# Kernel tuning notes

Hardware: AMD Instinct MI355X
Metric: run time of the kernel (lower is better)

The kernel has to match this reference:

```python
import jax, jax.numpy as jnp
import numpy as np

N, E, T, D, A = 16384, 65536, 2048, 64, 6


def _w(k, shape, fan_in):
    return jax.random.normal(k, shape, jnp.float32) / np.sqrt(fan_in)


def setup_inputs() -> dict:
    key = jax.random.key(0)
    ks = jax.random.split(key, 20)
    inp = {}
    inp["x"] = jax.random.normal(ks[0], (N, 3), jnp.float32)
    inp["edge_attr"] = jax.random.normal(ks[1], (E, 7), jnp.float32)
    inp["edge_index"] = jax.random.randint(ks[2], (2, E), 0, N)
    inp["nonring"] = jax.random.randint(ks[3], (T, 4), 0, N)
    inp["hx"] = jnp.zeros((1, D), jnp.float32)
    inp["cx"] = jnp.zeros((1, D), jnp.float32)
    inp["W_lin0"] = _w(ks[4], (D, 3), 3); inp["b_lin0"] = jnp.zeros((D,), jnp.float32)
    inp["W_e1"] = _w(ks[5], (128, 7), 7); inp["b_e1"] = jnp.zeros((128,), jnp.float32)
    inp["W_e2"] = _w(ks[6], (D * D, 128), 128); inp["b_e2"] = jnp.zeros((D * D,), jnp.float32)
    inp["conv_root"] = _w(ks[7], (D, D), D); inp["conv_bias"] = jnp.zeros((D,), jnp.float32)
    inp["gru_Wih"] = _w(ks[8], (3 * D, D), D); inp["gru_Whh"] = _w(ks[9], (3 * D, D), D)
    inp["gru_bih"] = jnp.zeros((3 * D,), jnp.float32); inp["gru_bhh"] = jnp.zeros((3 * D,), jnp.float32)
    inp["s2s_Wih"] = _w(ks[10], (4 * D, 2 * D), 2 * D); inp["s2s_Whh"] = _w(ks[11], (4 * D, D), D)
    inp["s2s_bih"] = jnp.zeros((4 * D,), jnp.float32); inp["s2s_bhh"] = jnp.zeros((4 * D,), jnp.float32)
    inp["mem_Wih"] = _w(ks[12], (4 * D, 2 * D), 2 * D); inp["mem_Whh"] = _w(ks[13], (4 * D, D), D)
    inp["mem_bih"] = jnp.zeros((4 * D,), jnp.float32); inp["mem_bhh"] = jnp.zeros((4 * D,), jnp.float32)
    inp["W_lin1"] = _w(ks[14], (D, 5 * D), 5 * D); inp["b_lin1"] = jnp.zeros((D,), jnp.float32)
    inp["W_lin2"] = _w(ks[15], (A, D), D); inp["b_lin2"] = jnp.zeros((A,), jnp.float32)
    inp["W_lin3"] = _w(ks[16], (1, 3 * D), 3 * D); inp["b_lin3"] = jnp.zeros((1,), jnp.float32)
    return inp


def _lstm_cell(xin, h, c, Wih, Whh, bih, bhh):
    g = xin @ Wih.T + bih + h @ Whh.T + bhh
    i, f, gg, o = jnp.split(g, 4, axis=-1)  # torch gate order i,f,g,o
    c = jax.nn.sigmoid(f) * c + jax.nn.sigmoid(i) * jnp.tanh(gg)
    h = jax.nn.sigmoid(o) * jnp.tanh(c)
    return h, c


def _gru_cell(xin, h, Wih, Whh, bih, bhh):
    gi = xin @ Wih.T + bih
    gh = h @ Whh.T + bhh
    ir, iz, inn = jnp.split(gi, 3, axis=-1)  # torch gate order r,z,n
    hr, hz, hn = jnp.split(gh, 3, axis=-1)
    r = jax.nn.sigmoid(ir + hr)
    z = jax.nn.sigmoid(iz + hz)
    n = jnp.tanh(inn + r * hn)
    return (1.0 - z) * n + z * h


def reference(x, edge_attr, edge_index, nonring, hx, cx,
              W_lin0, b_lin0, W_e1, b_e1, W_e2, b_e2, conv_root, conv_bias,
              gru_Wih, gru_Whh, gru_bih, gru_bhh,
              s2s_Wih, s2s_Whh, s2s_bih, s2s_bhh,
              mem_Wih, mem_Whh, mem_bih, mem_bhh,
              W_lin1, b_lin1, W_lin2, b_lin2, W_lin3, b_lin3):
    src, tgt = edge_index[0], edge_index[1]
    out = jax.nn.relu(x @ W_lin0.T + b_lin0)  # [N, D]
    h = out  # GRU hidden (nodes as batch)
    # edge-conditioned dim x dim matrices (NNConv edge MLP)
    ew = jax.nn.relu(edge_attr @ W_e1.T + b_e1)
    ew = (ew @ W_e2.T + b_e2).reshape(E, D, D)  # [E, D, D]
    cnt = jnp.maximum(jax.ops.segment_sum(jnp.ones((E,), out.dtype), tgt, num_segments=N), 1.0)
    for _ in range(3):
        msg = jnp.einsum('ed,edf->ef', out[src], ew)  # per-edge small matmul
        aggr = jax.ops.segment_sum(msg, tgt, num_segments=N) / cnt[:, None]  # scatter-mean
        m = jax.nn.relu(aggr + out @ conv_root + conv_bias)  # NNConv root + bias, then relu
        h = _gru_cell(m, h, gru_Wih, gru_Whh, gru_bih, gru_bhh)
        out = h
    # Set2Set pooling (single graph, B=1), processing_steps=3
    hs = jnp.zeros((1, D), out.dtype)
    cs = jnp.zeros((1, D), out.dtype)
    q_star = jnp.zeros((1, 2 * D), out.dtype)
    for _ in range(3):
        hs, cs = _lstm_cell(q_star, hs, cs, s2s_Wih, s2s_Whh, s2s_bih, s2s_bhh)
        a = jax.nn.softmax(out @ hs[0])  # [N]
        r = (a[:, None] * out).sum(0, keepdims=True)  # [1, D]
        q_star = jnp.concatenate([hs, r], axis=1)
    pool = q_star  # [1, 2D]
    lstm_out, cx_new = _lstm_cell(pool, hx, cx, mem_Wih, mem_Whh, mem_bih, mem_bhh)
    hx_new = lstm_out
    # torsion head: index_select -> view(4*D, -1) -> permute(1,0)
    sel = out[nonring.reshape(-1)]  # [4T, D]
    tfeat = sel.reshape(4 * D, -1).T  # [T, 4D], faithful to torch view semantics
    rep = jnp.repeat(lstm_out.reshape(-1), T).reshape(T, D)  # torch repeat_interleave + view
    pf = jnp.concatenate([tfeat, rep], axis=1)  # [T, 5D]
    logits = jax.nn.relu(pf @ W_lin1.T + b_lin1) @ W_lin2.T + b_lin2  # [T, A]
    v = jnp.concatenate([pool, lstm_out], axis=1) @ W_lin3.T + b_lin3  # [1, 1]
    return logits, v, hx_new, cx_new
```

## Files before the change

kernel.cpp:

```cpp
#include <hip/hip_runtime.h>

#define cN 16384
#define cE 65536
#define cT 2048
#define CAP 78

typedef __attribute__((ext_vector_type(8))) short short8;
typedef __attribute__((ext_vector_type(4))) float f32x4;
typedef __attribute__((ext_vector_type(4))) unsigned u32x4;

__device__ __forceinline__ short f2bf(float f){
  unsigned u = __float_as_uint(f);
  u = (u + 0x7FFFu + ((u >> 16) & 1u)) >> 16;
  return (short)u;
}
__device__ __forceinline__ float bf2f(short s){
  return __uint_as_float(((unsigned)(unsigned short)s) << 16);
}
__device__ __forceinline__ unsigned cvtpk(float lo, float hi){
  unsigned r;
  asm("v_cvt_pk_bf16_f32 %0, %1, %2" : "=v"(r) : "v"(lo), "v"(hi));
  return r;
}
__device__ __forceinline__ float sigm(float x){ return 1.f / (1.f + __expf(-x)); }
__device__ __forceinline__ unsigned fenc(float f){
  unsigned u = __float_as_uint(f);
  return (u & 0x80000000u) ? ~u : (u | 0x80000000u);
}
__device__ __forceinline__ float fdec(unsigned u){
  u = (u & 0x80000000u) ? (u & 0x7FFFFFFFu) : ~u;
  return __uint_as_float(u);
}
__device__ __forceinline__ float wred(float v){
  v += __shfl_xor(v, 32); v += __shfl_xor(v, 16); v += __shfl_xor(v, 8);
  v += __shfl_xor(v, 4);  v += __shfl_xor(v, 2);  v += __shfl_xor(v, 1);
  return v;
}

__global__ __launch_bounds__(256) void k_lin0(const float* __restrict__ x,
    const float* __restrict__ W, const float* __restrict__ b, float* __restrict__ out)
{
  int i = blockIdx.x * 256 + threadIdx.x;
  int n = i >> 6, f = i & 63;
  float acc = b[f] + x[n*3]*W[f*3] + x[n*3+1]*W[f*3+1] + x[n*3+2]*W[f*3+2];
  out[i] = fmaxf(acc, 0.f);
}

__global__ __launch_bounds__(256) void k_h1(const float* __restrict__ ea,
    const float* __restrict__ W, const float* __restrict__ b, short* __restrict__ h1)
{
  int i = blockIdx.x * 256 + threadIdx.x;
  int e = i >> 7, k = i & 127;
  const float* a = ea + e * 7;
  const float* w = W + k * 7;
  float acc = b[k];
  #pragma unroll
  for (int c = 0; c < 7; c++) acc += a[c] * w[c];
  h1[i] = f2bf(fmaxf(acc, 0.f));
}

__global__ __launch_bounds__(256) void k_w2f(const float* __restrict__ W2, short* __restrict__ w2f)
{
  int o = blockIdx.x * 256 + threadIdx.x;
  int j = o & 7, l = (o >> 3) & 63, ks = (o >> 9) & 31, c = (o >> 14) & 7, fb = (o >> 17) & 3;
  int f = fb * 16 + (l & 15);
  int d = c * 8 + j;
  int k = ks * 4 + ((l >> 4) & 3);
  w2f[o] = f2bf(W2[(d * 64 + f) * 128 + k]);
}

__global__ __launch_bounds__(256) void k_b2f(const float* __restrict__ b2, short* __restrict__ b2f)
{
  int o = blockIdx.x * 256 + threadIdx.x;
  int j = o & 7, l = (o >> 3) & 63, ks2 = (o >> 9) & 1, fb = (o >> 10) & 3;
  int d = ks2 * 32 + ((l >> 4) & 3) * 8 + j;
  int f = fb * 16 + (l & 15);
  b2f[o] = f2bf(b2[d * 64 + f]);
}

__global__ __launch_bounds__(256) void k_wpack(const float* __restrict__ convW,
    const float* __restrict__ Wih, const float* __restrict__ Whh, short* __restrict__ wpk)
{
  int o = blockIdx.x * 256 + threadIdx.x;
  int j = o & 7, l = (o >> 3) & 63, kc = (o >> 9) & 1, cb = o >> 10;
  int k = kc * 32 + ((l >> 4) & 3) * 8 + j;
  int c16 = l & 15;
  float v;
  if (cb < 4)       v = convW[k * 64 + cb * 16 + c16];
  else if (cb < 16) v = Wih[((cb - 4) * 16 + c16) * 64 + k];
  else              v = Whh[((cb - 16) * 16 + c16) * 64 + k];
  wpk[o] = f2bf(v);
}

__global__ __launch_bounds__(256) void k_deg(const int* __restrict__ ei, int* __restrict__ deg)
{
  int e = blockIdx.x * 256 + threadIdx.x;
  atomicAdd(&deg[ei[cE + e]], 1);
}

__global__ __launch_bounds__(1024) void k_scan(const int* __restrict__ deg,
    int* __restrict__ rowp, float* __restrict__ cnt)
{
  __shared__ int part[1024];
  int tid = threadIdx.x;
  int base = tid * 16;
  int loc[16]; int s = 0;
  #pragma unroll
  for (int i = 0; i < 16; i++){ loc[i] = s; s += deg[base + i]; }
  part[tid] = s;
  __syncthreads();
  for (int off = 1; off < 1024; off <<= 1){
    int v = (tid >= off) ? part[tid - off] : 0;
    __syncthreads();
    part[tid] += v;
    __syncthreads();
  }
  int inc = part[tid];
  int eb = inc - s;
  #pragma unroll
  for (int i = 0; i < 16; i++){
    rowp[base + i] = eb + loc[i];
    int dv = deg[base + i];
    cnt[base + i] = (float)(dv > 0 ? dv : 1);
  }
  if (tid == 1023) rowp[16384] = inc;
}

__global__ __launch_bounds__(256) void k_scatter(const int* __restrict__ ei,
    const int* __restrict__ rowp, int* __restrict__ cur,
    int* __restrict__ esrc, int* __restrict__ eidx)
{
  int e = blockIdx.x * 256 + threadIdx.x;
  int t = ei[cE + e];
  int pos = rowp[t] + atomicAdd(&cur[t], 1);
  esrc[pos] = ei[e];
  eidx[pos] = e;
}

__global__ __launch_bounds__(256) void k_sagg(const float* __restrict__ out,
    const short* __restrict__ h1, const short* __restrict__ w2f,
    const short* __restrict__ b2f, const int* __restrict__ rowp,
    const int* __restrict__ esrc, const int* __restrict__ eidx,
    float* __restrict__ aggr)
{
  __shared__ __align__(16) short S[16][1040];
  __shared__ __align__(16) unsigned h1i[CAP][64];
  __shared__ __align__(16) float outsf[CAP][64];
  __shared__ __align__(16) short osb[16][72];
  int tid = threadIdx.x, w = tid >> 6, lane = tid & 63;
  int t0 = blockIdx.x * 16;

  int ebase = rowp[t0];
  int eend  = rowp[t0 + 16];
  int ecnt  = eend - ebase;
  bool fits = (ecnt <= CAP);
  int scnt  = fits ? ecnt : CAP;
  for (int i = w; i < scnt; i += 4){
    int eid = eidx[ebase + i];
    int src = esrc[ebase + i];
    unsigned lo = (unsigned short)h1[(size_t)eid * 128 + lane];
    unsigned hi = (unsigned short)h1[(size_t)eid * 128 + 64 + lane];
    h1i[i][lane] = lo | (hi << 16);
    outsf[i][lane] = out[(size_t)src * 64 + lane];
  }
  int toff[4], tcnt[4];
  #pragma unroll
  for (int g = 0; g < 4; g++){
    int t = t0 + w * 4 + g;
    int a = rowp[t], b = rowp[t + 1];
    toff[g] = a - ebase; tcnt[g] = b - a;
  }
  __syncthreads();

  #pragma unroll
  for (int g = 0; g < 4; g++){
    int ti = w * 4 + g;
    float os = 0.f;
    int tf = toff[g], tc = tcnt[g];
    for (int p = 0; p < tc; p++){
      int slot = tf + p;
      if (slot < CAP) os += outsf[slot][lane];
      else            os += out[(size_t)esrc[ebase + slot] * 64 + lane];
    }
    osb[ti][lane] = (short)cvtpk(os, os);
  }

  f32x4 acc = {0.f, 0.f, 0.f, 0.f};
  int arow = lane & 15, kg = lane >> 4;
  for (int c = 0; c < 8; ++c){
    #pragma unroll
    for (int g = 0; g < 4; ++g){
      int ti = w * 4 + g;
      float a0[8], a1[8];
      #pragma unroll
      for (int d = 0; d < 8; d++){ a0[d] = 0.f; a1[d] = 0.f; }
      int tc = tcnt[g], tf = toff[g];
      if (fits){
        #pragma unroll 2
        for (int p = 0; p < tc; ++p){
          int slot = tf + p;
          unsigned u = h1i[slot][lane];
          float h1a = __uint_as_float(u << 16);
          float h1b = __uint_as_float(u & 0xFFFF0000u);
          f32x4 o0 = *(const f32x4*)&outsf[slot][c * 8];
          f32x4 o1 = *(const f32x4*)&outsf[slot][c * 8 + 4];
          a0[0] = fmaf(o0[0], h1a, a0[0]); a1[0] = fmaf(o0[0], h1b, a1[0]);
          a0[1] = fmaf(o0[1], h1a, a0[1]); a1[1] = fmaf(o0[1], h1b, a1[1]);
          a0[2] = fmaf(o0[2], h1a, a0[2]); a1[2] = fmaf(o0[2], h1b, a1[2]);
          a0[3] = fmaf(o0[3], h1a, a0[3]); a1[3] = fmaf(o0[3], h1b, a1[3]);
          a0[4] = fmaf(o1[0], h1a, a0[4]); a1[4] = fmaf(o1[0], h1b, a1[4]);
          a0[5] = fmaf(o1[1], h1a, a0[5]); a1[5] = fmaf(o1[1], h1b, a1[5]);
          a0[6] = fmaf(o1[2], h1a, a0[6]); a1[6] = fmaf(o1[2], h1b, a1[6]);
          a0[7] = fmaf(o1[3], h1a, a0[7]); a1[7] = fmaf(o1[3], h1b, a1[7]);
        }
      } else {
        for (int p = 0; p < tc; ++p){
          int slot = tf + p;
          float h1a, h1b;
          if (slot < CAP){
            unsigned u = h1i[slot][lane];
            h1a = __uint_as_float(u << 16);
            h1b = __uint_as_float(u & 0xFFFF0000u);
            f32x4 o0 = *(const f32x4*)&outsf[slot][c * 8];
            f32x4 o1 = *(const f32x4*)&outsf[slot][c * 8 + 4];
            #pragma unroll
            for (int d = 0; d < 4; d++){
              a0[d] = fmaf(o0[d], h1a, a0[d]); a1[d] = fmaf(o0[d], h1b, a1[d]);
              a0[4+d] = fmaf(o1[d], h1a, a0[4+d]); a1[4+d] = fmaf(o1[d], h1b, a1[4+d]);
            }
          } else {
            int eid = eidx[ebase + slot];
            int src = esrc[ebase + slot];
            h1a = bf2f(h1[(size_t)eid * 128 + lane]);
            h1b = bf2f(h1[(size_t)eid * 128 + 64 + lane]);
            #pragma unroll
            for (int d = 0; d < 8; d++){
              float o = out[(size_t)src * 64 + c * 8 + d];
              a0[d] = fmaf(o, h1a, a0[d]); a1[d] = fmaf(o, h1b, a1[d]);
            }
          }
        }
      }
      u32x4 p0, p1;
      p0[0] = cvtpk(a0[0], a0[1]); p0[1] = cvtpk(a0[2], a0[3]);
      p0[2] = cvtpk(a0[4], a0[5]); p0[3] = cvtpk(a0[6], a0[7]);
      p1[0] = cvtpk(a1[0], a1[1]); p1[1] = cvtpk(a1[2], a1[3]);
      p1[2] = cvtpk(a1[4], a1[5]); p1[3] = cvtpk(a1[6], a1[7]);
      *(u32x4*)&S[ti][lane * 8]       = p0;
      *(u32x4*)&S[ti][512 + lane * 8] = p1;
    }
    __syncthreads();
    const short* bbase = w2f + ((size_t)(w * 8 + c) * 32) * 512 + lane * 8;
    #pragma unroll
    for (int ks = 0; ks < 32; ++ks){
      short8 afr = *(const short8*)&S[arow][ks * 32 + kg * 8];
      short8 bfr = *(const short8*)(bbase + (size_t)ks * 512);
      acc = __builtin_amdgcn_mfma_f32_16x16x32_bf16(afr, bfr, acc, 0, 0, 0);
    }
    __syncthreads();
  }
  #pragma unroll
  for (int ks2 = 0; ks2 < 2; ++ks2){
    short8 osf = *(const short8*)&osb[arow][ks2 * 32 + kg * 8];
    short8 bfr = *(const short8*)(b2f + ((size_t)((w * 2 + ks2) * 64 + lane)) * 8);
    acc = __builtin_amdgcn_mfma_f32_16x16x32_bf16(osf, bfr, acc, 0, 0, 0);
  }
  int fcol = w * 16 + arow;
  int trow = kg * 4;
  #pragma unroll
  for (int q = 0; q < 4; q++)
    aggr[(size_t)(t0 + trow + q) * 64 + fcol] = acc[q];
}

__global__ __launch_bounds__(256) void k_nodeM(float* __restrict__ out,
    const float* __restrict__ aggr, const float* __restrict__ cnt,
    const short* __restrict__ wpk, const float* __restrict__ convB,
    const float* __restrict__ bih, const float* __restrict__ bhh)
{
  __shared__ __align__(16) short outA[64][72];
  __shared__ __align__(16) short mA[64][72];
  __shared__ float sb[448];
  const short8* WF = (const short8*)wpk;
  int tid = threadIdx.x, w = tid >> 6, lane = tid & 63;
  int n0 = blockIdx.x * 64;
  for (int i = tid; i < 2048; i += 256){
    int r = i >> 5, c2 = (i & 31) * 2;
    float2 v = *(const float2*)&out[(size_t)(n0 + r) * 64 + c2];
    *(unsigned*)&outA[r][c2] = cvtpk(v.x, v.y);
  }
  if (tid < 64) sb[tid] = convB[tid];
  for (int i = tid; i < 192; i += 256){ sb[64 + i] = bih[i]; sb[256 + i] = bhh[i]; }
  __syncthreads();
  int arow = lane & 15, kg = lane >> 4;
  int r0 = w * 16;
  short8 aof0 = *(const short8*)&outA[r0 + arow][kg * 8];
  short8 aof1 = *(const short8*)&outA[r0 + arow][32 + kg * 8];
  float ic[4];
  #pragma unroll
  for (int q = 0; q < 4; q++)
    ic[q] = 1.0f / fmaxf(cnt[n0 + r0 + kg * 4 + q], 1.0f);
  #pragma unroll
  for (int cf = 0; cf < 4; cf++){
    f32x4 a = {0.f, 0.f, 0.f, 0.f};
    a = __builtin_amdgcn_mfma_f32_16x16x32_bf16(aof0, WF[(cf * 2 + 0) * 64 + lane], a, 0, 0, 0);
    a = __builtin_amdgcn_mfma_f32_16x16x32_bf16(aof1, WF[(cf * 2 + 1) * 64 + lane], a, 0, 0, 0);
    int col = cf * 16 + arow;
    float cb_ = sb[col];
    #pragma unroll
    for (int q = 0; q < 4; q++){
      int r = n0 + r0 + kg * 4 + q;
      float m = fmaxf(aggr[(size_t)r * 64 + col] * ic[q] + a[q] + cb_, 0.f);
      mA[r0 + kg * 4 + q][col] = f2bf(m);
    }
  }
  __syncthreads();
  short8 amf0 = *(const short8*)&mA[r0 + arow][kg * 8];
  short8 amf1 = *(const short8*)&mA[r0 + arow][32 + kg * 8];
  #pragma unroll
  for (int co = 0; co < 4; co++){
    f32x4 gir = {0,0,0,0}, giz = {0,0,0,0}, gin = {0,0,0,0};
    f32x4 ghr = {0,0,0,0}, ghz = {0,0,0,0}, ghn = {0,0,0,0};
    gir = __builtin_amdgcn_mfma_f32_16x16x32_bf16(amf0, WF[((4  + co) * 2 + 0) * 64 + lane], gir, 0, 0, 0);
    gir = __builtin_amdgcn_mfma_f32_16x16x32_bf16(amf1, WF[((4  + co) * 2 + 1) * 64 + lane], gir, 0, 0, 0);
    giz = __builtin_amdgcn_mfma_f32_16x16x32_bf16(amf0, WF[((8  + co) * 2 + 0) * 64 + lane], giz, 0, 0, 0);
    giz = __builtin_amdgcn_mfma_f32_16x16x32_bf16(amf1, WF[((8  + co) * 2 + 1) * 64 + lane], giz, 0, 0, 0);
    gin = __builtin_amdgcn_mfma_f32_16x16x32_bf16(amf0, WF[((12 + co) * 2 + 0) * 64 + lane], gin, 0, 0, 0);
    gin = __builtin_amdgcn_mfma_f32_16x16x32_bf16(amf1, WF[((12 + co) * 2 + 1) * 64 + lane], gin, 0, 0, 0);
    ghr = __builtin_amdgcn_mfma_f32_16x16x32_bf16(aof0, WF[((16 + co) * 2 + 0) * 64 + lane], ghr, 0, 0, 0);
    ghr = __builtin_amdgcn_mfma_f32_16x16x32_bf16(aof1, WF[((16 + co) * 2 + 1) * 64 + lane], ghr, 0, 0, 0);
    ghz = __builtin_amdgcn_mfma_f32_16x16x32_bf16(aof0, WF[((20 + co) * 2 + 0) * 64 + lane], ghz, 0, 0, 0);
    ghz = __builtin_amdgcn_mfma_f32_16x16x32_bf16(aof1, WF[((20 + co) * 2 + 1) * 64 + lane], ghz, 0, 0, 0);
    ghn = __builtin_amdgcn_mfma_f32_16x16x32_bf16(aof0, WF[((24 + co) * 2 + 0) * 64 + lane], ghn, 0, 0, 0);
    ghn = __builtin_amdgcn_mfma_f32_16x16x32_bf16(aof1, WF[((24 + co) * 2 + 1) * 64 + lane], ghn, 0, 0, 0);
    int col = co * 16 + arow;
    float bir = sb[64 + col],  biz = sb[128 + col], bin_ = sb[192 + col];
    float bhr = sb[256 + col], bhz = sb[320 + col], bhn = sb[384 + col];
    #pragma unroll
    for (int q = 0; q < 4; q++){
      size_t r = (size_t)(n0 + r0 + kg * 4 + q);
      float rr = sigm(gir[q] + bir + ghr[q] + bhr);
      float zz = sigm(giz[q] + biz + ghz[q] + bhz);
      float nn = tanhf(gin[q] + bin_ + rr * (ghn[q] + bhn));
      float o = out[r * 64 + col];
      out[r * 64 + col] = (1.f - zz) * nn + zz * o;
    }
  }
}

__global__ __launch_bounds__(256) void k_dotsF(const float* __restrict__ out,
    const float* __restrict__ Wih, const float* __restrict__ Whh,
    const float* __restrict__ bih, const float* __restrict__ bhh,
    float* __restrict__ scal, float* __restrict__ sbuf, int st)
{
  __shared__ float q[128];
  __shared__ float hsL[64];
  __shared__ float gsh[4][64];
  __shared__ float hsh[64];
  __shared__ float smax[4];
  const float* pg = scal + st * 256;
  float* pn = scal + (st + 1) * 256;
  int tid = threadIdx.x, gg = tid >> 6, lane = tid & 63;
  if (gg == 0){
    float hs = pg[lane];
    float es = pg[193];
    float rv = (es == 0.f) ? 0.f : pg[128 + lane] / es;
    q[lane] = hs; q[64 + lane] = rv; hsL[lane] = hs;
  }
  __syncthreads();
  float2 fq = *(const float2*)&q[2 * lane];
  float hv0 = hsL[lane];
  #pragma unroll 4
  for (int o = 0; o < 64; o++){
    int row = gg * 64 + o;
    float2 wv = *(const float2*)&Wih[(size_t)row * 128 + 2 * lane];
    float s = wv.x * fq.x + wv.y * fq.y + Whh[(size_t)row * 64 + lane] * hv0;
    s = wred(s);
    if (lane == 0) gsh[gg][o] = s;
  }
  __syncthreads();
  if (gg == 0){
    float gi = gsh[0][lane] + bih[lane]       + bhh[lane];
    float gf = gsh[1][lane] + bih[64 + lane]  + bhh[64 + lane];
    float gv = gsh[2][lane] + bih[128 + lane] + bhh[128 + lane];
    float go = gsh[3][lane] + bih[192 + lane] + bhh[192 + lane];
    float cs = pg[64 + lane];
    float cn = sigm(gf) * cs + sigm(gi) * tanhf(gv);
    float hn = sigm(go) * tanhf(cn);
    hsh[lane] = hn;
    if (blockIdx.x == 0){ pn[lane] = hn; pn[64 + lane] = cn; }
  }
  __syncthreads();
  int nbase = blockIdx.x * 64 + gg * 16;
  float hv = hsh[lane];
  float wmax = -3.4e38f;
  #pragma unroll 4
  for (int i = 0; i < 16; i++){
    int n = nbase + i;
    float p = wred(out[(size_t)n * 64 + lane] * hv);
    if (lane == 0) sbuf[n] = p;
    wmax = fmaxf(wmax, p);
  }
  if (lane == 0) smax[gg] = wmax;
  __syncthreads();
  if (tid == 0){
    float m = fmaxf(fmaxf(smax[0], smax[1]), fmaxf(smax[2], smax[3]));
    atomicMax((unsigned*)(pn + 192), fenc(m));
  }
}

__global__ __launch_bounds__(256) void k_smF(const float* __restrict__ out,
    const float* __restrict__ sbuf, float* __restrict__ scal, int st)
{
  float* pn = scal + (st + 1) * 256;
  __shared__ float ebuf[64];
  __shared__ float rpart[4][64];
  int tid = threadIdx.x, wid = tid >> 6, lane = tid & 63;
  float gm = fdec(((const unsigned*)pn)[192]);
  int n0 = blockIdx.x * 64;
  if (tid < 64) ebuf[tid] = __expf(sbuf[n0 + tid] - gm);
  __syncthreads();
  float racc = 0.f;
  #pragma unroll 4
  for (int i = 0; i < 16; i++){
    int idx = wid * 16 + i;
    racc += ebuf[idx] * out[(size_t)(n0 + idx) * 64 + lane];
  }
  rpart[wid][lane] = racc;
  __syncthreads();
  if (wid == 0){
    float rt = rpart[0][lane] + rpart[1][lane] + rpart[2][lane] + rpart[3][lane];
    atomicAdd(&pn[128 + lane], rt);
  } else if (wid == 1){
    float es = wred(ebuf[lane]);
    if (lane == 0) atomicAdd(&pn[193], es);
  }
}

__global__ __launch_bounds__(256) void k_memlstm(const float* __restrict__ Wih,
    const float* __restrict__ Whh, const float* __restrict__ bih,
    const float* __restrict__ bhh, const float* __restrict__ hx,
    const float* __restrict__ cx, const float* __restrict__ W3,
    const float* __restrict__ b3, float* __restrict__ scal, float* __restrict__ dout)
{
  __shared__ float pool[128];
  __shared__ float hxs[64];
  __shared__ float gsh[4][64];
  __shared__ float lob[64];
  const float* pg = scal + 3 * 256;
  int tid = threadIdx.x, gg = tid >> 6, lane = tid & 63;
  if (gg == 0){
    pool[lane] = pg[lane];
    pool[64 + lane] = pg[128 + lane] / pg[193];
    hxs[lane] = hx[lane];
  }
  __syncthreads();
  float2 fq = *(const float2*)&pool[2 * lane];
  float hv = hxs[lane];
  #pragma unroll 4
  for (int o = 0; o < 64; o++){
    int row = gg * 64 + o;
    float2 wv = *(const float2*)&Wih[(size_t)row * 128 + 2 * lane];
    float s = wv.x * fq.x + wv.y * fq.y + Whh[(size_t)row * 64 + lane] * hv;
    s = wred(s);
    if (lane == 0) gsh[gg][o] = s;
  }
  __syncthreads();
  if (gg == 0){
    float gi = gsh[0][lane] + bih[lane]       + bhh[lane];
    float gf = gsh[1][lane] + bih[64 + lane]  + bhh[64 + lane];
    float gv = gsh[2][lane] + bih[128 + lane] + bhh[128 + lane];
    float go = gsh[3][lane] + bih[192 + lane] + bhh[192 + lane];
    float cn = sigm(gf) * cx[lane] + sigm(gi) * tanhf(gv);
    float hn = sigm(go) * tanhf(cn);
    dout[12289 + lane] = hn;
    dout[12353 + lane] = cn;
    scal[1024 + lane] = hn;
    lob[lane] = hn;
  }
  __syncthreads();
  if (gg == 0){
    float a = pool[lane] * W3[lane] + pool[64 + lane] * W3[64 + lane]
            + lob[lane] * W3[128 + lane];
    a = wred(a);
    if (lane == 0) dout[12288] = a + b3[0];
  }
}

__global__ __launch_bounds__(256) void k_head(const float* __restrict__ out,
    const int* __restrict__ nr, const float* __restrict__ scal,
    const float* __restrict__ W1, const float* __restrict__ b1,
    const float* __restrict__ W2, const float* __restrict__ b2,
    float* __restrict__ dout)
{
  __shared__ float pf[4][320];
  __shared__ float hb[4][64];
  int tid = threadIdx.x, wid = tid >> 6, lane = tid & 63;
  int t = blockIdx.x * 4 + wid;
  float lo = scal[1024 + (t >> 5)];
  #pragma unroll
  for (int rep = 0; rep < 4; rep++){
    int j = rep * 64 + lane;
    int idx = nr[j * 32 + (t >> 6)];
    pf[wid][j] = out[idx * 64 + (t & 63)];
  }
  pf[wid][256 + lane] = lo;
  __syncthreads();
  float acc = b1[lane];
  const float* w = W1 + lane * 320;
  #pragma unroll 4
  for (int j = 0; j < 320; j++) acc += pf[wid][j] * w[j];
  hb[wid][lane] = fmaxf(acc, 0.f);
  __syncthreads();
  if (lane < 6){
    float a2 = b2[lane];
    const float* w2 = W2 + lane * 64;
    #pragma unroll 4
    for (int f = 0; f < 64; f++) a2 += hb[wid][f] * w2[f];
    dout[t * 6 + lane] = a2;
  }
}

extern "C" void kernel_launch(void* const* d_in, const int* in_sizes, int n_in,
                              void* d_out, int out_size, void* d_ws, size_t ws_size,
                              hipStream_t stream)
{
  const float* x         = (const float*)d_in[0];
  const float* edge_attr = (const float*)d_in[1];
  const int*   ei        = (const int*)d_in[2];
  const int*   nonring   = (const int*)d_in[3];
  const float* hx        = (const float*)d_in[4];
  const float* cx        = (const float*)d_in[5];
  const float* W_lin0 = (const float*)d_in[6];  const float* b_lin0 = (const float*)d_in[7];
  const float* W_e1   = (const float*)d_in[8];  const float* b_e1   = (const float*)d_in[9];
  const float* W_e2   = (const float*)d_in[10]; const float* b_e2   = (const float*)d_in[11];
  const float* convW  = (const float*)d_in[12]; const float* convB  = (const float*)d_in[13];
  const float* gWih   = (const float*)d_in[14]; const float* gWhh   = (const float*)d_in[15];
  const float* gbih   = (const float*)d_in[16]; const float* gbhh   = (const float*)d_in[17];
  const float* sWih   = (const float*)d_in[18]; const float* sWhh   = (const float*)d_in[19];
  const float* sbih   = (const float*)d_in[20]; const float* sbhh   = (const float*)d_in[21];
  const float* mWih   = (const float*)d_in[22]; const float* mWhh   = (const float*)d_in[23];
  const float* mbih   = (const float*)d_in[24]; const float* mbhh   = (const float*)d_in[25];
  const float* W_lin1 = (const float*)d_in[26]; const float* b_lin1 = (const float*)d_in[27];
  const float* W_lin2 = (const float*)d_in[28]; const float* b_lin2 = (const float*)d_in[29];
  const float* W_lin3 = (const float*)d_in[30]; const float* b_lin3 = (const float*)d_in[31];
  float* dout = (float*)d_out;

  char* w = (char*)d_ws;
  float* outb = (float*)w;  w += (size_t)cN * 64 * 4;
  float* aggr = (float*)w;  w += (size_t)cN * 64 * 4;
  short* h1   = (short*)w;  w += (size_t)cE * 128 * 2;
  short* w2f  = (short*)w;  w += (size_t)64 * 8192 * 2;
  short* b2f  = (short*)w;  w += 4096 * 2;
  short* wpk  = (short*)w;  w += 28672 * 2;
  float* cntb = (float*)w;  w += cN * 4;
  float* sbuf = (float*)w;  w += cN * 4;
  float* scal = (float*)w;  w += 1088 * 4;
  int* deg  = (int*)w;  w += cN * 4;
  int* cur  = (int*)w;  w += cN * 4;
  int* rowp = (int*)w;  w += (cN + 1) * 4 + 60;
  int* esrc = (int*)w;  w += cE * 4;
  int* eidx = (int*)w;  w += cE * 4;

  hipMemsetAsync(deg, 0, cN * 4, stream);
  hipMemsetAsync(cur, 0, cN * 4, stream);
  hipMemsetAsync(scal, 0, 1088 * 4, stream);

  k_lin0<<<cN * 64 / 256, 256, 0, stream>>>(x, W_lin0, b_lin0, outb);
  k_h1<<<cE * 128 / 256, 256, 0, stream>>>(edge_attr, W_e1, b_e1, h1);
  k_w2f<<<64 * 8192 / 256, 256, 0, stream>>>(W_e2, w2f);
  k_b2f<<<16, 256, 0, stream>>>(b_e2, b2f);
  k_wpack<<<112, 256, 0, stream>>>(convW, gWih, gWhh, wpk);
  k_deg<<<cE / 256, 256, 0, stream>>>(ei, deg);
  k_scan<<<1, 1024, 0, stream>>>(deg, rowp, cntb);
  k_scatter<<<cE / 256, 256, 0, stream>>>(ei, rowp, cur, esrc, eidx);

  for (int it = 0; it < 3; it++){
    k_sagg<<<cN / 16, 256, 0, stream>>>(outb, h1, w2f, b2f, rowp, esrc, eidx, aggr);
    k_nodeM<<<cN / 64, 256, 0, stream>>>(outb, aggr, cntb, wpk, convB, gbih, gbhh);
  }

  for (int st = 0; st < 3; st++){
    k_dotsF<<<cN / 64, 256, 0, stream>>>(outb, sWih, sWhh, sbih, sbhh, scal, sbuf, st);
    k_smF<<<cN / 64, 256, 0, stream>>>(outb, sbuf, scal, st);
  }

  k_memlstm<<<1, 256, 0, stream>>>(mWih, mWhh, mbih, mbhh, hx, cx, W_lin3, b_lin3, scal, dout);
  k_head<<<cT / 4, 256, 0, stream>>>(outb, nonring, scal, W_lin1, b_lin1, W_lin2, b_lin2, dout);
}
```

Baseline: 601.4 us.

## Fuse setup kernels, double-buffer sagg LDS, and restructure Set2Set softmax as per-block partials

Merges the six setup kernels (lin0, h1, w2f, b2f, wpack, deg) into one block-range-dispatched launch to cut launch overhead. In k_sagg the staging tile S is double-buffered by chunk parity, which removes the trailing barrier per chunk, and the neighbour cache CAP grows from 78 to 88. Set2Set pooling now writes per-block max, exp-sum and weighted sums instead of using global atomics and a separate softmax kernel. The next step's kernel, or a final one that also does the memory LSTM, combines these partials. This cuts kernel count and atomics but adds more LDS per block (occupancy risk) and redundant 256-way reductions in every block.

```diff
diff --git a/kernel.cpp b/kernel.cpp
--- a/kernel.cpp
+++ b/kernel.cpp
@@ -3,7 +3,7 @@
 #define cN 16384
 #define cE 65536
 #define cT 2048
-#define CAP 78
+#define CAP 88
 
 typedef __attribute__((ext_vector_type(8))) short short8;
 typedef __attribute__((ext_vector_type(4))) float f32x4;
@@ -23,79 +23,77 @@
   return r;
 }
 __device__ __forceinline__ float sigm(float x){ return 1.f / (1.f + __expf(-x)); }
-__device__ __forceinline__ unsigned fenc(float f){
-  unsigned u = __float_as_uint(f);
-  return (u & 0x80000000u) ? ~u : (u | 0x80000000u);
-}
-__device__ __forceinline__ float fdec(unsigned u){
-  u = (u & 0x80000000u) ? (u & 0x7FFFFFFFu) : ~u;
-  return __uint_as_float(u);
-}
 __device__ __forceinline__ float wred(float v){
   v += __shfl_xor(v, 32); v += __shfl_xor(v, 16); v += __shfl_xor(v, 8);
   v += __shfl_xor(v, 4);  v += __shfl_xor(v, 2);  v += __shfl_xor(v, 1);
   return v;
 }
-
-__global__ __launch_bounds__(256) void k_lin0(const float* __restrict__ x,
-    const float* __restrict__ W, const float* __restrict__ b, float* __restrict__ out)
-{
-  int i = blockIdx.x * 256 + threadIdx.x;
-  int n = i >> 6, f = i & 63;
-  float acc = b[f] + x[n*3]*W[f*3] + x[n*3+1]*W[f*3+1] + x[n*3+2]*W[f*3+2];
-  out[i] = fmaxf(acc, 0.f);
-}
-
-__global__ __launch_bounds__(256) void k_h1(const float* __restrict__ ea,
-    const float* __restrict__ W, const float* __restrict__ b, short* __restrict__ h1)
-{
-  int i = blockIdx.x * 256 + threadIdx.x;
-  int e = i >> 7, k = i & 127;
-  const float* a = ea + e * 7;
-  const float* w = W + k * 7;
-  float acc = b[k];
-  #pragma unroll
-  for (int c = 0; c < 7; c++) acc += a[c] * w[c];
-  h1[i] = f2bf(fmaxf(acc, 0.f));
-}
-
-__global__ __launch_bounds__(256) void k_w2f(const float* __restrict__ W2, short* __restrict__ w2f)
-{
-  int o = blockIdx.x * 256 + threadIdx.x;
-  int j = o & 7, l = (o >> 3) & 63, ks = (o >> 9) & 31, c = (o >> 14) & 7, fb = (o >> 17) & 3;
-  int f = fb * 16 + (l & 15);
-  int d = c * 8 + j;
-  int k = ks * 4 + ((l >> 4) & 3);
-  w2f[o] = f2bf(W2[(d * 64 + f) * 128 + k]);
-}
-
-__global__ __launch_bounds__(256) void k_b2f(const float* __restrict__ b2, short* __restrict__ b2f)
-{
-  int o = blockIdx.x * 256 + threadIdx.x;
-  int j = o & 7, l = (o >> 3) & 63, ks2 = (o >> 9) & 1, fb = (o >> 10) & 3;
-  int d = ks2 * 32 + ((l >> 4) & 3) * 8 + j;
-  int f = fb * 16 + (l & 15);
-  b2f[o] = f2bf(b2[d * 64 + f]);
-}
-
-__global__ __launch_bounds__(256) void k_wpack(const float* __restrict__ convW,
-    const float* __restrict__ Wih, const float* __restrict__ Whh, short* __restrict__ wpk)
-{
-  int o = blockIdx.x * 256 + threadIdx.x;
-  int j = o & 7, l = (o >> 3) & 63, kc = (o >> 9) & 1, cb = o >> 10;
-  int k = kc * 32 + ((l >> 4) & 3) * 8 + j;
-  int c16 = l & 15;
-  float v;
-  if (cb < 4)       v = convW[k * 64 + cb * 16 + c16];
-  else if (cb < 16) v = Wih[((cb - 4) * 16 + c16) * 64 + k];
-  else              v = Whh[((cb - 16) * 16 + c16) * 64 + k];
-  wpk[o] = f2bf(v);
-}
-
-__global__ __launch_bounds__(256) void k_deg(const int* __restrict__ ei, int* __restrict__ deg)
-{
-  int e = blockIdx.x * 256 + threadIdx.x;
-  atomicAdd(&deg[ei[cE + e]], 1);
+__device__ __forceinline__ float wredmax(float v){
+  v = fmaxf(v, __shfl_xor(v, 32)); v = fmaxf(v, __shfl_xor(v, 16));
+  v = fmaxf(v, __shfl_xor(v, 8));  v = fmaxf(v, __shfl_xor(v, 4));
+  v = fmaxf(v, __shfl_xor(v, 2));  v = fmaxf(v, __shfl_xor(v, 1));
+  return v;
+}
+
+#define B_L0   4096
+#define B_H1   36864
+#define B_W2   38912
+#define B_B2   38928
+#define B_WP   39040
+#define B_DEG  39296
+__global__ __launch_bounds__(256) void k_setup(
+    const float* __restrict__ x, const float* __restrict__ Wl0, const float* __restrict__ bl0,
+    float* __restrict__ out,
+    const float* __restrict__ ea, const float* __restrict__ We1, const float* __restrict__ be1,
+    short* __restrict__ h1,
+    const float* __restrict__ W2, short* __restrict__ w2f,
+    const float* __restrict__ b2, short* __restrict__ b2f,
+    const float* __restrict__ convW, const float* __restrict__ gWih,
+    const float* __restrict__ gWhh, short* __restrict__ wpk,
+    const int* __restrict__ ei, int* __restrict__ deg)
+{
+  int b = blockIdx.x, tid = threadIdx.x;
+  if (b < B_L0){
+    int i = b * 256 + tid;
+    int n = i >> 6, f = i & 63;
+    float acc = bl0[f] + x[n*3]*Wl0[f*3] + x[n*3+1]*Wl0[f*3+1] + x[n*3+2]*Wl0[f*3+2];
+    out[i] = fmaxf(acc, 0.f);
+  } else if (b < B_H1){
+    int i = (b - B_L0) * 256 + tid;
+    int e = i >> 7, k = i & 127;
+    const float* a = ea + e * 7;
+    const float* w = We1 + k * 7;
+    float acc = be1[k];
+    #pragma unroll
+    for (int c = 0; c < 7; c++) acc += a[c] * w[c];
+    h1[i] = f2bf(fmaxf(acc, 0.f));
+  } else if (b < B_W2){
+    int o = (b - B_H1) * 256 + tid;
+    int j = o & 7, l = (o >> 3) & 63, ks = (o >> 9) & 31, c = (o >> 14) & 7, fb = (o >> 17) & 3;
+    int f = fb * 16 + (l & 15);
+    int d = c * 8 + j;
+    int k = ks * 4 + ((l >> 4) & 3);
+    w2f[o] = f2bf(W2[(d * 64 + f) * 128 + k]);
+  } else if (b < B_B2){
+    int o = (b - B_W2) * 256 + tid;
+    int j = o & 7, l = (o >> 3) & 63, ks2 = (o >> 9) & 1, fb = (o >> 10) & 3;
+    int d = ks2 * 32 + ((l >> 4) & 3) * 8 + j;
+    int f = fb * 16 + (l & 15);
+    b2f[o] = f2bf(b2[d * 64 + f]);
+  } else if (b < B_WP){
+    int o = (b - B_B2) * 256 + tid;
+    int j = o & 7, l = (o >> 3) & 63, kc = (o >> 9) & 1, cb = o >> 10;
+    int k = kc * 32 + ((l >> 4) & 3) * 8 + j;
+    int c16 = l & 15;
+    float v;
+    if (cb < 4)       v = convW[k * 64 + cb * 16 + c16];
+    else if (cb < 16) v = gWih[((cb - 4) * 16 + c16) * 64 + k];
+    else              v = gWhh[((cb - 16) * 16 + c16) * 64 + k];
+    wpk[o] = f2bf(v);
+  } else {
+    int e = (b - B_WP) * 256 + tid;
+    atomicAdd(&deg[ei[cE + e]], 1);
+  }
 }
 
 __global__ __launch_bounds__(1024) void k_scan(const int* __restrict__ deg,
@@ -143,7 +141,7 @@
     const int* __restrict__ esrc, const int* __restrict__ eidx,
     float* __restrict__ aggr)
 {
-  __shared__ __align__(16) short S[16][1040];
+  __shared__ __align__(16) short S[2][16][1040];
   __shared__ __align__(16) unsigned h1i[CAP][64];
   __shared__ __align__(16) float outsf[CAP][64];
   __shared__ __align__(16) short osb[16][72];
@@ -188,6 +186,7 @@
   f32x4 acc = {0.f, 0.f, 0.f, 0.f};
   int arow = lane & 15, kg = lane >> 4;
   for (int c = 0; c < 8; ++c){
+    int buf = c & 1;
     #pragma unroll
     for (int g = 0; g < 4; ++g){
       int ti = w * 4 + g;
@@ -216,11 +215,10 @@
       } else {
         for (int p = 0; p < tc; ++p){
           int slot = tf + p;
-          float h1a, h1b;
           if (slot < CAP){
             unsigned u = h1i[slot][lane];
-            h1a = __uint_as_float(u << 16);
-            h1b = __uint_as_float(u & 0xFFFF0000u);
+            float h1a = __uint_as_float(u << 16);
+            float h1b = __uint_as_float(u & 0xFFFF0000u);
             f32x4 o0 = *(const f32x4*)&outsf[slot][c * 8];
             f32x4 o1 = *(const f32x4*)&outsf[slot][c * 8 + 4];
             #pragma unroll
@@ -231,8 +229,8 @@
           } else {
             int eid = eidx[ebase + slot];
             int src = esrc[ebase + slot];
-            h1a = bf2f(h1[(size_t)eid * 128 + lane]);
-            h1b = bf2f(h1[(size_t)eid * 128 + 64 + lane]);
+            float h1a = bf2f(h1[(size_t)eid * 128 + lane]);
+            float h1b = bf2f(h1[(size_t)eid * 128 + 64 + lane]);
             #pragma unroll
             for (int d = 0; d < 8; d++){
               float o = out[(size_t)src * 64 + c * 8 + d];
@@ -246,18 +244,17 @@
       p0[2] = cvtpk(a0[4], a0[5]); p0[3] = cvtpk(a0[6], a0[7]);
       p1[0] = cvtpk(a1[0], a1[1]); p1[1] = cvtpk(a1[2], a1[3]);
       p1[2] = cvtpk(a1[4], a1[5]); p1[3] = cvtpk(a1[6], a1[7]);
-      *(u32x4*)&S[ti][lane * 8]       = p0;
-      *(u32x4*)&S[ti][512 + lane * 8] = p1;
+      *(u32x4*)&S[buf][ti][lane * 8]       = p0;
+      *(u32x4*)&S[buf][ti][512 + lane * 8] = p1;
     }
     __syncthreads();
     const short* bbase = w2f + ((size_t)(w * 8 + c) * 32) * 512 + lane * 8;
     #pragma unroll
     for (int ks = 0; ks < 32; ++ks){
-      short8 afr = *(const short8*)&S[arow][ks * 32 + kg * 8];
+      short8 afr = *(const short8*)&S[buf][arow][ks * 32 + kg * 8];
       short8 bfr = *(const short8*)(bbase + (size_t)ks * 512);
       acc = __builtin_amdgcn_mfma_f32_16x16x32_bf16(afr, bfr, acc, 0, 0, 0);
     }
-    __syncthreads();
   }
   #pragma unroll
   for (int ks2 = 0; ks2 < 2; ++ks2){
@@ -350,22 +347,45 @@
 __global__ __launch_bounds__(256) void k_dotsF(const float* __restrict__ out,
     const float* __restrict__ Wih, const float* __restrict__ Whh,
     const float* __restrict__ bih, const float* __restrict__ bhh,
-    float* __restrict__ scal, float* __restrict__ sbuf, int st)
+    float* __restrict__ scal,
+    const float* __restrict__ rbI, const float* __restrict__ bmI, const float* __restrict__ esI,
+    float* __restrict__ rbO, float* __restrict__ bmO, float* __restrict__ esO, int st)
 {
   __shared__ float q[128];
   __shared__ float hsL[64];
   __shared__ float gsh[4][64];
   __shared__ float hsh[64];
   __shared__ float smax[4];
+  __shared__ float otile[64][64];
+  __shared__ float sarr[64];
+  __shared__ float ebuf[64];
+  __shared__ float rpart[4][64];
+  __shared__ float redA[4], redB[4];
   const float* pg = scal + st * 256;
   float* pn = scal + (st + 1) * 256;
   int tid = threadIdx.x, gg = tid >> 6, lane = tid & 63;
-  if (gg == 0){
-    float hs = pg[lane];
-    float es = pg[193];
-    float rv = (es == 0.f) ? 0.f : pg[128 + lane] / es;
-    q[lane] = hs; q[64 + lane] = rv; hsL[lane] = hs;
-  }
+  if (st > 0){
+    float bm = bmI[tid];
+    float m = wredmax(bm);
+    if (lane == 0) redA[gg] = m;
+    __syncthreads();
+    float gmax = fmaxf(fmaxf(redA[0], redA[1]), fmaxf(redA[2], redA[3]));
+    float ep = wred(__expf(bm - gmax) * esI[tid]);
+    if (lane == 0) redB[gg] = ep;
+    float racc = 0.f;
+    for (int i = 0; i < 64; i++){
+      int b = gg * 64 + i;
+      racc += __expf(bmI[b] - gmax) * rbI[b * 64 + lane];
+    }
+    rpart[gg][lane] = racc;
+    __syncthreads();
+    if (gg == 0){
+      float esum = redB[0] + redB[1] + redB[2] + redB[3];
+      float r = rpart[0][lane] + rpart[1][lane] + rpart[2][lane] + rpart[3][lane];
+      q[64 + lane] = r / esum;
+    }
+  } else if (gg == 0) q[64 + lane] = 0.f;
+  if (gg == 0){ float hs = pg[lane]; q[lane] = hs; hsL[lane] = hs; }
   __syncthreads();
   float2 fq = *(const float2*)&q[2 * lane];
   float hv0 = hsL[lane];
@@ -395,62 +415,66 @@
   float wmax = -3.4e38f;
   #pragma unroll 4
   for (int i = 0; i < 16; i++){
-    int n = nbase + i;
-    float p = wred(out[(size_t)n * 64 + lane] * hv);
-    if (lane == 0) sbuf[n] = p;
+    float v = out[(size_t)(nbase + i) * 64 + lane];
+    otile[gg * 16 + i][lane] = v;
+    float p = wred(v * hv);
+    if (lane == 0) sarr[gg * 16 + i] = p;
     wmax = fmaxf(wmax, p);
   }
   if (lane == 0) smax[gg] = wmax;
   __syncthreads();
-  if (tid == 0){
-    float m = fmaxf(fmaxf(smax[0], smax[1]), fmaxf(smax[2], smax[3]));
-    atomicMax((unsigned*)(pn + 192), fenc(m));
-  }
-}
-
-__global__ __launch_bounds__(256) void k_smF(const float* __restrict__ out,
-    const float* __restrict__ sbuf, float* __restrict__ scal, int st)
-{
-  float* pn = scal + (st + 1) * 256;
-  __shared__ float ebuf[64];
-  __shared__ float rpart[4][64];
-  int tid = threadIdx.x, wid = tid >> 6, lane = tid & 63;
-  float gm = fdec(((const unsigned*)pn)[192]);
-  int n0 = blockIdx.x * 64;
-  if (tid < 64) ebuf[tid] = __expf(sbuf[n0 + tid] - gm);
+  float bm = fmaxf(fmaxf(smax[0], smax[1]), fmaxf(smax[2], smax[3]));
+  if (tid < 64) ebuf[tid] = __expf(sarr[tid] - bm);
   __syncthreads();
   float racc = 0.f;
   #pragma unroll 4
-  for (int i = 0; i < 16; i++){
-    int idx = wid * 16 + i;
-    racc += ebuf[idx] * out[(size_t)(n0 + idx) * 64 + lane];
-  }
-  rpart[wid][lane] = racc;
-  __syncthreads();
-  if (wid == 0){
-    float rt = rpart[0][lane] + rpart[1][lane] + rpart[2][lane] + rpart[3][lane];
-    atomicAdd(&pn[128 + lane], rt);
-  } else if (wid == 1){
+  for (int i = 0; i < 16; i++)
+    racc += ebuf[gg * 16 + i] * otile[gg * 16 + i][lane];
+  rpart[gg][lane] = racc;
+  __syncthreads();
+  if (gg == 0){
+    float r = rpart[0][lane] + rpart[1][lane] + rpart[2][lane] + rpart[3][lane];
+    rbO[blockIdx.x * 64 + lane] = r;
+  } else if (gg == 1){
     float es = wred(ebuf[lane]);
-    if (lane == 0) atomicAdd(&pn[193], es);
-  }
-}
-
-__global__ __launch_bounds__(256) void k_memlstm(const float* __restrict__ Wih,
-    const float* __restrict__ Whh, const float* __restrict__ bih,
-    const float* __restrict__ bhh, const float* __restrict__ hx,
-    const float* __restrict__ cx, const float* __restrict__ W3,
-    const float* __restrict__ b3, float* __restrict__ scal, float* __restrict__ dout)
-{
+    if (lane == 0) esO[blockIdx.x] = es;
+  } else if (gg == 2 && lane == 0) bmO[blockIdx.x] = bm;
+}
+
+__global__ __launch_bounds__(256) void k_smFin(
+    const float* __restrict__ rbI, const float* __restrict__ bmI, const float* __restrict__ esI,
+    const float* __restrict__ Wih, const float* __restrict__ Whh,
+    const float* __restrict__ bih, const float* __restrict__ bhh,
+    const float* __restrict__ hx, const float* __restrict__ cx,
+    const float* __restrict__ W3, const float* __restrict__ b3,
+    float* __restrict__ scal, float* __restrict__ dout)
+{
+  __shared__ float redA[4], redB[4];
+  __shared__ float rpart[4][64];
   __shared__ float pool[128];
   __shared__ float hxs[64];
   __shared__ float gsh[4][64];
   __shared__ float lob[64];
-  const float* pg = scal + 3 * 256;
-  int tid = threadIdx.x, gg = tid >> 6, lane = tid & 63;
-  if (gg == 0){
-    pool[lane] = pg[lane];
-    pool[64 + lane] = pg[128 + lane] / pg[193];
+  int tid = threadIdx.x, wid = tid >> 6, lane = tid & 63;
+  float bm = bmI[tid];
+  float m = wredmax(bm);
+  if (lane == 0) redA[wid] = m;
+  __syncthreads();
+  float gmax = fmaxf(fmaxf(redA[0], redA[1]), fmaxf(redA[2], redA[3]));
+  float ep = wred(__expf(bm - gmax) * esI[tid]);
+  if (lane == 0) redB[wid] = ep;
+  float racc = 0.f;
+  for (int i = 0; i < 64; i++){
+    int b = wid * 64 + i;
+    racc += __expf(bmI[b] - gmax) * rbI[b * 64 + lane];
+  }
+  rpart[wid][lane] = racc;
+  __syncthreads();
+  if (wid == 0){
+    float esum = redB[0] + redB[1] + redB[2] + redB[3];
+    float r = rpart[0][lane] + rpart[1][lane] + rpart[2][lane] + rpart[3][lane];
+    pool[lane] = scal[3 * 256 + lane];
+    pool[64 + lane] = r / esum;
     hxs[lane] = hx[lane];
   }
   __syncthreads();
@@ -458,14 +482,14 @@
   float hv = hxs[lane];
   #pragma unroll 4
   for (int o = 0; o < 64; o++){
-    int row = gg * 64 + o;
+    int row = wid * 64 + o;
     float2 wv = *(const float2*)&Wih[(size_t)row * 128 + 2 * lane];
     float s = wv.x * fq.x + wv.y * fq.y + Whh[(size_t)row * 64 + lane] * hv;
     s = wred(s);
-    if (lane == 0) gsh[gg][o] = s;
-  }
-  __syncthreads();
-  if (gg == 0){
+    if (lane == 0) gsh[wid][o] = s;
+  }
+  __syncthreads();
+  if (wid == 0){
     float gi = gsh[0][lane] + bih[lane]       + bhh[lane];
     float gf = gsh[1][lane] + bih[64 + lane]  + bhh[64 + lane];
     float gv = gsh[2][lane] + bih[128 + lane] + bhh[128 + lane];
@@ -478,7 +502,7 @@
     lob[lane] = hn;
   }
   __syncthreads();
-  if (gg == 0){
+  if (wid == 0){
     float a = pool[lane] * W3[lane] + pool[64 + lane] * W3[64 + lane]
             + lob[lane] * W3[128 + lane];
     a = wred(a);
@@ -553,7 +577,12 @@
   short* b2f  = (short*)w;  w += 4096 * 2;
   short* wpk  = (short*)w;  w += 28672 * 2;
   float* cntb = (float*)w;  w += cN * 4;
-  float* sbuf = (float*)w;  w += cN * 4;
+  float* rbufA= (float*)w;  w += 256 * 64 * 4;
+  float* rbufB= (float*)w;  w += 256 * 64 * 4;
+  float* bmA  = (float*)w;  w += 256 * 4;
+  float* bmB  = (float*)w;  w += 256 * 4;
+  float* esA  = (float*)w;  w += 256 * 4;
+  float* esB  = (float*)w;  w += 256 * 4;
   float* scal = (float*)w;  w += 1088 * 4;
   int* deg  = (int*)w;  w += cN * 4;
   int* cur  = (int*)w;  w += cN * 4;
@@ -565,12 +594,9 @@
   hipMemsetAsync(cur, 0, cN * 4, stream);
   hipMemsetAsync(scal, 0, 1088 * 4, stream);
 
-  k_lin0<<<cN * 64 / 256, 256, 0, stream>>>(x, W_lin0, b_lin0, outb);
-  k_h1<<<cE * 128 / 256, 256, 0, stream>>>(edge_attr, W_e1, b_e1, h1);
-  k_w2f<<<64 * 8192 / 256, 256, 0, stream>>>(W_e2, w2f);
-  k_b2f<<<16, 256, 0, stream>>>(b_e2, b2f);
-  k_wpack<<<112, 256, 0, stream>>>(convW, gWih, gWhh, wpk);
-  k_deg<<<cE / 256, 256, 0, stream>>>(ei, deg);
+  k_setup<<<B_DEG, 256, 0, stream>>>(x, W_lin0, b_lin0, outb,
+      edge_attr, W_e1, b_e1, h1, W_e2, w2f, b_e2, b2f,
+      convW, gWih, gWhh, wpk, ei, deg);
   k_scan<<<1, 1024, 0, stream>>>(deg, rowp, cntb);
   k_scatter<<<cE / 256, 256, 0, stream>>>(ei, rowp, cur, esrc, eidx);
 
@@ -579,11 +605,14 @@
     k_nodeM<<<cN / 64, 256, 0, stream>>>(outb, aggr, cntb, wpk, convB, gbih, gbhh);
   }
 
-  for (int st = 0; st < 3; st++){
-    k_dotsF<<<cN / 64, 256, 0, stream>>>(outb, sWih, sWhh, sbih, sbhh, scal, sbuf, st);
-    k_smF<<<cN / 64, 256, 0, stream>>>(outb, sbuf, scal, st);
-  }
-
-  k_memlstm<<<1, 256, 0, stream>>>(mWih, mWhh, mbih, mbhh, hx, cx, W_lin3, b_lin3, scal, dout);
+  k_dotsF<<<cN / 64, 256, 0, stream>>>(outb, sWih, sWhh, sbih, sbhh, scal,
+      rbufA, bmA, esA, rbufA, bmA, esA, 0);
+  k_dotsF<<<cN / 64, 256, 0, stream>>>(outb, sWih, sWhh, sbih, sbhh, scal,
+      rbufA, bmA, esA, rbufB, bmB, esB, 1);
+  k_dotsF<<<cN / 64, 256, 0, stream>>>(outb, sWih, sWhh, sbih, sbhh, scal,
+      rbufB, bmB, esB, rbufA, bmA, esA, 2);
+  k_smFin<<<1, 256, 0, stream>>>(rbufA, bmA, esA,
+      mWih, mWhh, mbih, mbhh, hx, cx, W_lin3, b_lin3, scal, dout);
+
   k_head<<<cT / 4, 256, 0, stream>>>(outb, nonring, scal, W_lin1, b_lin1, W_lin2, b_lin2, dout);
 }
```

Result: slower. 663.3 us (+10.3%).
